# Kernel optimization log

Hardware: AMD Instinct MI355X
Metric: run time of the kernel (lower is better)

Reference implementation:

```python
import jax, jax.numpy as jnp
import numpy as np

N_NODES = 100000
IN_F = 128
H_F = 128
LOOKBACK = 3
N_EDGES = 640000


def setup_inputs() -> dict:
    key = jax.random.key(0)
    ks = jax.random.split(key, 16)
    s = lambda k, shp: jax.random.normal(k, shp, dtype=jnp.float32) * 0.05
    inp = {
        "feat": jax.random.normal(ks[0], (N_NODES, IN_F), dtype=jnp.float32),
        "edges": jax.random.randint(ks[1], (LOOKBACK, 2, N_EDGES), 0, N_NODES, dtype=jnp.int32),
        # conv1 (SAGEConv pool, in->h) params
        "Wp1": s(ks[2], (IN_F, IN_F)), "bp1": jnp.zeros((IN_F,), jnp.float32),
        "Ws1": s(ks[3], (H_F, IN_F)), "Wn1": s(ks[4], (H_F, IN_F)), "b1": jnp.zeros((H_F,), jnp.float32),
        # BatchNorm1d affine params (training-mode batch stats)
        "gamma": jnp.ones((H_F,), jnp.float32), "beta": jnp.zeros((H_F,), jnp.float32),
        # conv2 (SAGEConv pool, h->h) params
        "Wp2": s(ks[5], (H_F, H_F)), "bp2": jnp.zeros((H_F,), jnp.float32),
        "Ws2": s(ks[6], (H_F, H_F)), "Wn2": s(ks[7], (H_F, H_F)), "b2": jnp.zeros((H_F,), jnp.float32),
    }
    return inp


def _sage_pool_conv(h, src, dst, Wp, bp, Ws, Wn, b):
    # pool aggregator: m = relu(fc_pool(h)); neigh = max over in-edges
    m = jax.nn.relu(h @ Wp.T + bp)                      # [N, d]
    agg = jax.ops.segment_max(m[src], dst, num_segments=N_NODES)  # [N, d]
    agg = jnp.where(jnp.isfinite(agg), agg, 0.0)        # nodes with no in-edges -> 0
    return h @ Ws.T + agg @ Wn.T + b


def _batchnorm(x, gamma, beta, eps=1e-5):
    mu = jnp.mean(x, axis=0)
    var = jnp.var(x, axis=0)
    return (x - mu) * jax.lax.rsqrt(var + eps) * gamma + beta


def reference(feat, edges, Wp1, bp1, Ws1, Wn1, b1, gamma, beta, Wp2, bp2, Ws2, Wn2, b2):
    def per_graph(e):
        src, dst = e[0], e[1]
        h = _sage_pool_conv(feat, src, dst, Wp1, bp1, Ws1, Wn1, b1)
        h = _batchnorm(h, gamma, beta)
        h = jax.nn.relu(h)
        h = _sage_pool_conv(h, src, dst, Wp2, bp2, Ws2, Wn2, b2)
        return h

    return jax.vmap(per_graph)(edges)  # [lookback, N, H_F]
```

## Files before the change

### kernel.cpp

```cpp
#include <hip/hip_runtime.h>
#include <hip/hip_bf16.h>

#define NNODES 100000
#define FD 128
#define NEDGES 640000
#define NB 391
#define GRID64 1563
#define OFFS_U32 100032
#define BNRED 64

typedef __bf16 bf16x8 __attribute__((ext_vector_type(8)));
typedef __bf16 bf16x4 __attribute__((ext_vector_type(4)));
typedef float f32x4 __attribute__((ext_vector_type(4)));
typedef unsigned short u16x8 __attribute__((ext_vector_type(8)));

__device__ __forceinline__ bf16x8 cvt8(float4 a, float4 b) {
  bf16x8 r;
  r[0] = (__bf16)a.x; r[1] = (__bf16)a.y; r[2] = (__bf16)a.z; r[3] = (__bf16)a.w;
  r[4] = (__bf16)b.x; r[5] = (__bf16)b.y; r[6] = (__bf16)b.z; r[7] = (__bf16)b.w;
  return r;
}

__device__ __forceinline__ void gl16(const void* g, void* l) {
  __builtin_amdgcn_global_load_lds(
      (const __attribute__((address_space(1))) unsigned int*)g,
      (__attribute__((address_space(3))) unsigned int*)l, 16, 0, 0);
}

__device__ __forceinline__ void stage_w32(const __bf16* Wp, char* l, int tid) {
  const int wid = tid >> 6, lane = tid & 63;
#pragma unroll
  for (int i = 0; i < 8; ++i) {
    const int off = (wid * 8 + i) * 1024;
    gl16((const char*)Wp + off + lane * 16, l + off);
  }
}

__device__ __forceinline__ void stage_abf(const __bf16* A, long row0, int M,
                                          char* l, int tid) {
  const int wid = tid >> 6;
  long row = row0 + (tid & 63);
  if (row > M - 1) row = M - 1;
  const char* base = (const char*)(A + row * FD);
#pragma unroll
  for (int i = 0; i < 4; ++i) {
    const int s = wid * 4 + i;
    gl16(base + s * 16, l + s * 1024);
  }
}

__global__ __launch_bounds__(256) void packw6_k(
    const float* __restrict__ W0, const float* __restrict__ W1,
    const float* __restrict__ W2, const float* __restrict__ W3,
    const float* __restrict__ W4, const float* __restrict__ W5,
    __bf16* __restrict__ out) {
  const int gidx = blockIdx.x * 256 + threadIdx.x;
  const int wi = gidx >> 11;
  const int f = gidx & 2047;
  const float* W = wi == 0 ? W0 : wi == 1 ? W1 : wi == 2 ? W2
                 : wi == 3 ? W3 : wi == 4 ? W4 : W5;
  const int c = f >> 8, kk = (f >> 6) & 3, lane = f & 63;
  const int lr = lane & 15, lg = lane >> 4;
  const float* p = W + (c * 16 + lr) * FD + kk * 32 + lg * 8;
  *(bf16x8*)(out + (long)gidx * 8) = cvt8(*(const float4*)p, *(const float4*)(p + 4));
}

__device__ __forceinline__ void glb_arow32(const float* A, long row, int kbase,
                                           bf16x8 (&af)[4]) {
#pragma unroll
  for (int kk = 0; kk < 4; ++kk) {
    const float* ap = A + row * FD + kbase + kk * 32;
    af[kk] = cvt8(*(const float4*)ap, *(const float4*)(ap + 4));
  }
}

template <int AM>
__device__ __forceinline__ void lds_abf(const char* l, int rl, int lg,
                                        const float* __restrict__ scsh,
                                        bf16x8 (&af)[4]) {
#pragma unroll
  for (int kk = 0; kk < 4; ++kk) {
    const bf16x8 r = *(const bf16x8*)(l + (kk * 4 + lg) * 1024 + rl * 16);
    if constexpr (AM == 3) {
      const int k = lg * 8 + kk * 32;
      const float4 scx = *(const float4*)(scsh + k);
      const float4 scy = *(const float4*)(scsh + k + 4);
      const float4 shx = *(const float4*)(scsh + 128 + k);
      const float4 shy = *(const float4*)(scsh + 128 + k + 4);
      bf16x8 o;
      o[0] = (__bf16)fmaxf((float)r[0] * scx.x + shx.x, 0.f);
      o[1] = (__bf16)fmaxf((float)r[1] * scx.y + shx.y, 0.f);
      o[2] = (__bf16)fmaxf((float)r[2] * scx.z + shx.z, 0.f);
      o[3] = (__bf16)fmaxf((float)r[3] * scx.w + shx.w, 0.f);
      o[4] = (__bf16)fmaxf((float)r[4] * scy.x + shy.x, 0.f);
      o[5] = (__bf16)fmaxf((float)r[5] * scy.y + shy.y, 0.f);
      o[6] = (__bf16)fmaxf((float)r[6] * scy.z + shy.z, 0.f);
      o[7] = (__bf16)fmaxf((float)r[7] * scy.w + shy.w, 0.f);
      af[kk] = o;
    } else {
      af[kk] = r;
    }
  }
}

template <int A0M, int A1M, bool TWOA, bool RELU, bool OUTBF16, bool STATS, bool WRITEB>
__global__ __launch_bounds__(256, 2) void gemm_k(
    const void* __restrict__ A0, long a0s, const void* __restrict__ A1, long a1s,
    const __bf16* __restrict__ W0p, const __bf16* __restrict__ W1p,
    const float* __restrict__ bias, const float* __restrict__ scsh0,
    void* __restrict__ outp, long os, float* __restrict__ pblk,
    __bf16* __restrict__ bcopy, int M) {
  constexpr int LSZ = TWOA ? 65536 : (A0M == 0 ? 32768 : 49152);
  __shared__ __align__(16) char lds[LSZ];
  char* lW0 = lds;
  char* lA0 = lds + 32768;
  char* lA1 = lds + 49152;
  char* lW1 = lds + 32768;

  const int g = blockIdx.y;
  const int tid = threadIdx.x;
  const int wid = tid >> 6;
  const int lane = tid & 63;
  const int rw = wid & 1;
  const int cw = wid >> 1;
  const int lr = lane & 15;
  const int lg = lane >> 4;
  const long row0 = (long)blockIdx.x * 64;

  const void* A0g = (const char*)A0 + (long)g * a0s;
  const void* A1g = (const char*)A1 + (TWOA ? (long)g * a1s : 0);
  void* outg = (char*)outp + (long)g * os;
  const float* scshg = (A0M == 3 || A1M == 3) ? scsh0 + (long)g * 256 : nullptr;

  stage_w32(W0p, lW0, tid);
  if constexpr (A0M != 0) stage_abf((const __bf16*)A0g, row0, M, lA0, tid);
  if constexpr (TWOA) stage_abf((const __bf16*)A1g, row0, M, lA1, tid);
  __syncthreads();

  bf16x8 a0[2][4];
  bf16x8 a1[2][4];
  if constexpr (A0M == 0) {
#pragma unroll
    for (int t = 0; t < 2; ++t) {
      long row = row0 + rw * 32 + t * 16 + lr;
      if (row > M - 1) row = M - 1;
      glb_arow32((const float*)A0g, row, lg * 8, a0[t]);
    }
  } else {
#pragma unroll
    for (int t = 0; t < 2; ++t)
      lds_abf<A0M>(lA0, rw * 32 + t * 16 + lr, lg, scshg, a0[t]);
  }
  if constexpr (TWOA) {
#pragma unroll
    for (int t = 0; t < 2; ++t)
      lds_abf<A1M>(lA1, rw * 32 + t * 16 + lr, lg, scshg, a1[t]);
    __syncthreads();
    stage_w32(W1p, lW1, tid);
  }

  if constexpr (WRITEB) {
    if (cw == 0) {
#pragma unroll
      for (int t = 0; t < 2; ++t) {
        const long row = row0 + rw * 32 + t * 16 + lr;
        if (row < M)
#pragma unroll
          for (int kk = 0; kk < 4; ++kk)
            *(bf16x8*)(bcopy + row * FD + lg * 8 + kk * 32) = a0[t][kk];
      }
    }
  }

  f32x4 acc[2][4];
#pragma unroll
  for (int t = 0; t < 2; ++t)
#pragma unroll
    for (int ci = 0; ci < 4; ++ci) acc[t][ci] = (f32x4){0.f, 0.f, 0.f, 0.f};

#pragma unroll
  for (int ci = 0; ci < 4; ++ci) {
    bf16x8 bw[4];
#pragma unroll
    for (int kk = 0; kk < 4; ++kk)
      bw[kk] = *(const bf16x8*)(lW0 + ((cw * 4 + ci) * 4 + kk) * 1024 + lane * 16);
#pragma unroll
    for (int t = 0; t < 2; ++t)
#pragma unroll
      for (int kk = 0; kk < 4; ++kk)
        acc[t][ci] = __builtin_amdgcn_mfma_f32_16x16x32_bf16(bw[kk], a0[t][kk], acc[t][ci], 0, 0, 0);
  }
  if constexpr (TWOA) {
    __syncthreads();
#pragma unroll
    for (int ci = 0; ci < 4; ++ci) {
      bf16x8 bw[4];
#pragma unroll
      for (int kk = 0; kk < 4; ++kk)
        bw[kk] = *(const bf16x8*)(lW1 + ((cw * 4 + ci) * 4 + kk) * 1024 + lane * 16);
#pragma unroll
      for (int t = 0; t < 2; ++t)
#pragma unroll
        for (int kk = 0; kk < 4; ++kk)
          acc[t][ci] = __builtin_amdgcn_mfma_f32_16x16x32_bf16(bw[kk], a1[t][kk], acc[t][ci], 0, 0, 0);
    }
  }

  float ps[4][4], pss[4][4];
  if constexpr (STATS) {
#pragma unroll
    for (int ci = 0; ci < 4; ++ci)
#pragma unroll
      for (int j = 0; j < 4; ++j) { ps[ci][j] = 0.f; pss[ci][j] = 0.f; }
  }

#pragma unroll
  for (int t = 0; t < 2; ++t) {
    const long row = row0 + rw * 32 + t * 16 + lr;
    const bool ok = row < M;
#pragma unroll
    for (int ci = 0; ci < 4; ++ci) {
      const int cb = cw * 64 + ci * 16 + lg * 4;
      f32x4 v = acc[t][ci];
      if (bias) {
        const float4 bv = *(const float4*)(bias + cb);
        v[0] += bv.x; v[1] += bv.y; v[2] += bv.z; v[3] += bv.w;
      }
      if constexpr (STATS) {
        if (ok) {
#pragma unroll
          for (int j = 0; j < 4; ++j) { ps[ci][j] += v[j]; pss[ci][j] += v[j] * v[j]; }
        }
      }
      if constexpr (RELU) {
#pragma unroll
        for (int j = 0; j < 4; ++j) v[j] = fmaxf(v[j], 0.f);
      }
      if (ok) {
        if constexpr (OUTBF16) {
          bf16x4 o;
          o[0] = (__bf16)v[0]; o[1] = (__bf16)v[1];
          o[2] = (__bf16)v[2]; o[3] = (__bf16)v[3];
          *(bf16x4*)((__bf16*)outg + row * FD + cb) = o;
        } else {
          *(f32x4*)((float*)outg + row * FD + cb) = v;
        }
      }
    }
  }

  if constexpr (STATS) {
    __shared__ float s_red[2][4][64];
#pragma unroll
    for (int ci = 0; ci < 4; ++ci)
#pragma unroll
      for (int j = 0; j < 4; ++j) {
        float s = ps[ci][j], q = pss[ci][j];
        s += __shfl_xor(s, 1); s += __shfl_xor(s, 2);
        s += __shfl_xor(s, 4); s += __shfl_xor(s, 8);
        q += __shfl_xor(q, 1); q += __shfl_xor(q, 2);
        q += __shfl_xor(q, 4); q += __shfl_xor(q, 8);
        if (lr == 0) {
          s_red[0][wid][ci * 16 + lg * 4 + j] = s;
          s_red[1][wid][ci * 16 + lg * 4 + j] = q;
        }
      }
    __syncthreads();
    const int wh = tid >> 7, cg = tid & 127;
    const int cwi = cg >> 6, cl = cg & 63;
    float* pblkg = pblk + (long)g * ((long)GRID64 * 256);
    pblkg[(long)blockIdx.x * 256 + tid] =
        s_red[wh][cwi * 2 + 0][cl] + s_red[wh][cwi * 2 + 1][cl];
  }
}

__global__ __launch_bounds__(256) void bn_red1_k(const float* __restrict__ pblk,
                                                 float* __restrict__ pblk2) {
  const int g = blockIdx.y;
  const float* p = pblk + (long)g * GRID64 * 256;
  float s = 0.f;
  for (int r = blockIdx.x; r < GRID64; r += BNRED) s += p[(long)r * 256 + threadIdx.x];
  pblk2[((long)g * BNRED + blockIdx.x) * 256 + threadIdx.x] = s;
}

__global__ __launch_bounds__(256) void bn_final2_k(const float* __restrict__ pblk2,
                                                   const float* __restrict__ gamma,
                                                   const float* __restrict__ beta,
                                                   float* __restrict__ scsh3) {
  __shared__ float s_ss[128];
  const int g = blockIdx.y;
  const int tid = threadIdx.x;
  const float* p = pblk2 + (long)g * BNRED * 256;
  float s = 0.f;
#pragma unroll
  for (int r = 0; r < BNRED; ++r) s += p[r * 256 + tid];
  if (tid >= 128) s_ss[tid - 128] = s;
  __syncthreads();
  if (tid < 128) {
    const float mu = s / (float)NNODES;
    const float var = s_ss[tid] / (float)NNODES - mu * mu;
    const float sc = rsqrtf(var + 1e-5f) * gamma[tid];
    scsh3[g * 256 + tid] = sc;
    scsh3[g * 256 + 128 + tid] = beta[tid] - mu * sc;
  }
}


__global__ __launch_bounds__(256) void hist_rank3_k(const int* __restrict__ edges,
                                                    unsigned* __restrict__ deg3,
                                                    unsigned short* __restrict__ rank3) {
  const int g = blockIdx.y;
  const int e = blockIdx.x * 256 + threadIdx.x;
  if (e < NEDGES) {
    const int d = edges[(long)g * 2 * NEDGES + NEDGES + e];
    const unsigned r = atomicAdd(&deg3[(long)g * NNODES + d], 1u);
    rank3[(long)g * NEDGES + e] = (unsigned short)r;
  }
}

__global__ __launch_bounds__(256) void blocksum3_k(const unsigned* __restrict__ deg3,
                                                   unsigned* __restrict__ bsum3) {
  __shared__ unsigned s[256];
  const int g = blockIdx.y;
  const int i = blockIdx.x * 256 + threadIdx.x;
  s[threadIdx.x] = (i < NNODES) ? deg3[(long)g * NNODES + i] : 0u;
  __syncthreads();
#pragma unroll
  for (int o = 128; o > 0; o >>= 1) {
    if (threadIdx.x < o) s[threadIdx.x] += s[threadIdx.x + o];
    __syncthreads();
  }
  if (threadIdx.x == 0) bsum3[g * NB + blockIdx.x] = s[0];
}

__global__ __launch_bounds__(512) void scanb3_k(const unsigned* __restrict__ bsum3,
                                                unsigned* __restrict__ boffs3,
                                                unsigned* __restrict__ offs3) {
  __shared__ unsigned s[512];
  const int g = blockIdx.y;
  const unsigned v = (threadIdx.x < NB) ? bsum3[g * NB + threadIdx.x] : 0u;
  s[threadIdx.x] = v;
  __syncthreads();
#pragma unroll
  for (int o = 1; o < 512; o <<= 1) {
    unsigned t = (threadIdx.x >= o) ? s[threadIdx.x - o] : 0u;
    __syncthreads();
    s[threadIdx.x] += t;
    __syncthreads();
  }
  if (threadIdx.x < NB) boffs3[g * NB + threadIdx.x] = s[threadIdx.x] - v;
  if (threadIdx.x == 0) offs3[(long)g * OFFS_U32 + NNODES] = NEDGES;
}

__global__ __launch_bounds__(256) void offsets3_k(const unsigned* __restrict__ deg3,
                                                  const unsigned* __restrict__ boffs3,
                                                  unsigned* __restrict__ offs3) {
  __shared__ unsigned s[256];
  const int g = blockIdx.y;
  const int i = blockIdx.x * 256 + threadIdx.x;
  const unsigned v = (i < NNODES) ? deg3[(long)g * NNODES + i] : 0u;
  s[threadIdx.x] = v;
  __syncthreads();
#pragma unroll
  for (int o = 1; o < 256; o <<= 1) {
    unsigned t = (threadIdx.x >= o) ? s[threadIdx.x - o] : 0u;
    __syncthreads();
    s[threadIdx.x] += t;
    __syncthreads();
  }
  const unsigned excl = s[threadIdx.x] - v + boffs3[g * NB + blockIdx.x];
  if (i < NNODES) offs3[(long)g * OFFS_U32 + i] = excl;
}

__global__ __launch_bounds__(256) void scat3_k(const int* __restrict__ edges,
                                               const unsigned* __restrict__ offs3,
                                               const unsigned short* __restrict__ rank3,
                                               int* __restrict__ ssrc3) {
  const int g = blockIdx.y;
  const int e = blockIdx.x * 256 + threadIdx.x;
  if (e < NEDGES) {
    const int s = edges[(long)g * 2 * NEDGES + e];
    const int d = edges[(long)g * 2 * NEDGES + NEDGES + e];
    const unsigned p = offs3[(long)g * OFFS_U32 + d] + rank3[(long)g * NEDGES + e];
    ssrc3[(long)g * NEDGES + p] = s;
  }
}

__global__ __launch_bounds__(256) void agg_k(const unsigned short* __restrict__ m,
                                             long ms, const int* __restrict__ ssrc3,
                                             const unsigned* __restrict__ offs3,
                                             unsigned short* __restrict__ agg3) {
  const int g = blockIdx.y;
  const unsigned short* mg = m + (long)g * ms;
  const int* ssrc = ssrc3 + (long)g * NEDGES;
  const unsigned* offs = offs3 + (long)g * OFFS_U32;
  unsigned short* agg = agg3 + (long)g * NNODES * FD;

  const int gid = blockIdx.x * 256 + threadIdx.x;
  const int node = gid >> 4;
  if (node >= NNODES) return;
  const int fl = (gid & 15) * 8;
  const unsigned beg = offs[node], end = offs[node + 1];
  u16x8 acc = {0, 0, 0, 0, 0, 0, 0, 0};
  unsigned i = beg;
  for (; i + 2 <= end; i += 2) {
    const int s0 = ssrc[i];
    const int s1 = ssrc[i + 1];
    const u16x8 v0 = *(const u16x8*)(mg + (long)s0 * FD + fl);
    const u16x8 v1 = *(const u16x8*)(mg + (long)s1 * FD + fl);
#pragma unroll
    for (int j = 0; j < 8; ++j) {
      const unsigned short mx = v0[j] > v1[j] ? v0[j] : v1[j];
      acc[j] = mx > acc[j] ? mx : acc[j];
    }
  }
  if (i < end) {
    const u16x8 v = *(const u16x8*)(mg + (long)ssrc[i] * FD + fl);
#pragma unroll
    for (int j = 0; j < 8; ++j) acc[j] = v[j] > acc[j] ? v[j] : acc[j];
  }
  *(u16x8*)(agg + (long)node * FD + fl) = acc;
}

__global__ __launch_bounds__(256) void zero_k(float4* __restrict__ p, long n4) {
  const long i = (long)blockIdx.x * 256 + threadIdx.x;
  if (i < n4) p[i] = (float4){0.f, 0.f, 0.f, 0.f};
}

extern "C" void kernel_launch(void* const* d_in, const int* in_sizes, int n_in,
                              void* d_out, int out_size, void* d_ws, size_t ws_size,
                              hipStream_t stream) {
  const float* feat = (const float*)d_in[0];
  const int* edges = (const int*)d_in[1];
  const float* Wp1 = (const float*)d_in[2];
  const float* bp1 = (const float*)d_in[3];
  const float* Ws1 = (const float*)d_in[4];
  const float* Wn1 = (const float*)d_in[5];
  const float* b1 = (const float*)d_in[6];
  const float* gamma = (const float*)d_in[7];
  const float* beta = (const float*)d_in[8];
  const float* Wp2 = (const float*)d_in[9];
  const float* bp2 = (const float*)d_in[10];
  const float* Ws2 = (const float*)d_in[11];
  const float* Wn2 = (const float*)d_in[12];
  const float* b2 = (const float*)d_in[13];

  const long SZ_BF = 25600000;
  const long SZ_F32 = 51200000;

  char* w = (char*)d_ws;
  __bf16* m1 = (__bf16*)w;
  __bf16* featb = (__bf16*)(w + 25600000);
  __bf16* h1b3 = (__bf16*)(w + 51200000);
  __bf16* aggb3 = (__bf16*)(w + 128000000);
  __bf16* m2_3 = (__bf16*)(w + 204800000);
  float* pblk3 = (float*)(w + 204800000);
  float* pblk2_3 = (float*)(w + 209700096);
  __bf16* wpk = (__bf16*)(w + 281600000);
  float* scsh3 = (float*)(w + 281796608);
  unsigned* deg3 = (unsigned*)(w + 281799680);
  unsigned* offs3 = (unsigned*)(w + 282999680);
  unsigned* bsum3 = (unsigned*)(w + 284200064);
  unsigned* boffs3 = (unsigned*)(w + 284204928);
  unsigned short* rank3 = (unsigned short*)(w + 284209792);
  int* ssrc3 = (int*)(w + 288049792);

  __bf16* Wp1p = wpk;
  __bf16* Ws1p = wpk + 16384;
  __bf16* Wn1p = wpk + 2 * 16384;
  __bf16* Wp2p = wpk + 3 * 16384;
  __bf16* Ws2p = wpk + 4 * 16384;
  __bf16* Wn2p = wpk + 5 * 16384;

  const dim3 blk(256);
  const int edgeGrid = (NEDGES + 255) / 256;
  const int aggGrid = (NNODES * 16 + 255) / 256;
  const int degZeroGrid = (3 * NNODES / 4 + 255) / 256;

  packw6_k<<<48, blk, 0, stream>>>(Wp1, Ws1, Wn1, Wp2, Ws2, Wn2, wpk);

  zero_k<<<degZeroGrid, blk, 0, stream>>>((float4*)deg3, 3L * NNODES / 4);
  hist_rank3_k<<<dim3(edgeGrid, 3), blk, 0, stream>>>(edges, deg3, rank3);
  blocksum3_k<<<dim3(NB, 3), blk, 0, stream>>>(deg3, bsum3);
  scanb3_k<<<dim3(1, 3), dim3(512), 0, stream>>>(bsum3, boffs3, offs3);
  offsets3_k<<<dim3(NB, 3), blk, 0, stream>>>(deg3, boffs3, offs3);
  scat3_k<<<dim3(edgeGrid, 3), blk, 0, stream>>>(edges, offs3, rank3, ssrc3);

  gemm_k<0, 0, false, true, true, false, true><<<dim3(GRID64, 1), blk, 0, stream>>>(
      feat, 0, nullptr, 0, Wp1p, nullptr, bp1, nullptr, m1, 0, nullptr, featb, NNODES);

  agg_k<<<dim3(aggGrid, 3), blk, 0, stream>>>((const unsigned short*)m1, 0L,
                                              ssrc3, offs3, (unsigned short*)aggb3);
  gemm_k<1, 1, true, false, true, true, false><<<dim3(GRID64, 3), blk, 0, stream>>>(
      aggb3, SZ_BF, featb, 0, Wn1p, Ws1p, b1, nullptr, h1b3, SZ_BF, pblk3, nullptr, NNODES);
  bn_red1_k<<<dim3(BNRED, 3), blk, 0, stream>>>(pblk3, pblk2_3);
  bn_final2_k<<<dim3(1, 3), blk, 0, stream>>>(pblk2_3, gamma, beta, scsh3);

  gemm_k<3, 0, false, true, true, false, false><<<dim3(GRID64, 3), blk, 0, stream>>>(
      h1b3, SZ_BF, nullptr, 0, Wp2p, nullptr, bp2, scsh3, m2_3, SZ_BF, nullptr, nullptr, NNODES);
  agg_k<<<dim3(aggGrid, 3), blk, 0, stream>>>((const unsigned short*)m2_3,
                                              (long)NNODES * FD, ssrc3, offs3,
                                              (unsigned short*)aggb3);
  gemm_k<3, 1, true, false, false, false, false><<<dim3(GRID64, 3), blk, 0, stream>>>(
      h1b3, SZ_BF, aggb3, SZ_BF, Ws2p, Wn2p, b2, scsh3, d_out, SZ_F32, nullptr, nullptr, NNODES);
}
```

Before: 556.9 us.

## Make GEMM kernels persistent with double-buffered A tiles and resident weights

The GEMM kernels become persistent 512-thread blocks. Each block stages the weights into LDS once and then loops over 64-row tiles with a grid stride, prefetching the next A tile into a second LDS buffer via global_load_lds while computing the current one. The head GEMM now stages fp32 features through LDS rather than loading them straight from global memory. With fewer blocks, the BatchNorm partial sums come from 85 blocks per graph and the intermediate reduction kernel is removed. The cost is a large LDS footprint at one block per CU and a barrier on every tile.

```diff
diff --git a/kernel.cpp b/kernel.cpp
--- a/kernel.cpp
+++ b/kernel.cpp
@@ -5,9 +5,11 @@
 #define FD 128
 #define NEDGES 640000
 #define NB 391
-#define GRID64 1563
+#define NT64 1563
+#define GX_TWOA 85
+#define GX_ONEW 170
+#define GX_HEAD 255
 #define OFFS_U32 100032
-#define BNRED 64
 
 typedef __bf16 bf16x8 __attribute__((ext_vector_type(8)));
 typedef __bf16 bf16x4 __attribute__((ext_vector_type(4)));
@@ -27,19 +29,29 @@
       (__attribute__((address_space(3))) unsigned int*)l, 16, 0, 0);
 }
 
-__device__ __forceinline__ void stage_w32(const __bf16* Wp, char* l, int tid) {
-  const int wid = tid >> 6, lane = tid & 63;
-#pragma unroll
-  for (int i = 0; i < 8; ++i) {
-    const int off = (wid * 8 + i) * 1024;
+__device__ __forceinline__ void stage_w32(const __bf16* Wp, char* l, int wid, int lane) {
+#pragma unroll
+  for (int i = 0; i < 4; ++i) {
+    const int off = (wid * 4 + i) * 1024;
     gl16((const char*)Wp + off + lane * 16, l + off);
   }
 }
 
 __device__ __forceinline__ void stage_abf(const __bf16* A, long row0, int M,
-                                          char* l, int tid) {
-  const int wid = tid >> 6;
-  long row = row0 + (tid & 63);
+                                          char* l, int wid, int lane) {
+  long row = row0 + lane;
+  if (row > M - 1) row = M - 1;
+  const char* base = (const char*)(A + row * FD);
+#pragma unroll
+  for (int i = 0; i < 2; ++i) {
+    const int s = wid * 2 + i;
+    gl16(base + s * 16, l + s * 1024);
+  }
+}
+
+__device__ __forceinline__ void stage_a32(const float* A, long row0, int M,
+                                          char* l, int wid, int lane) {
+  long row = row0 + lane;
   if (row > M - 1) row = M - 1;
   const char* base = (const char*)(A + row * FD);
 #pragma unroll
@@ -65,163 +77,141 @@
   *(bf16x8*)(out + (long)gidx * 8) = cvt8(*(const float4*)p, *(const float4*)(p + 4));
 }
 
-__device__ __forceinline__ void glb_arow32(const float* A, long row, int kbase,
-                                           bf16x8 (&af)[4]) {
+template <int AM>
+__device__ __forceinline__ void lds_arow(const char* l, int rl, int lg,
+                                         const float* __restrict__ scsh,
+                                         bf16x8 (&af)[4]) {
 #pragma unroll
   for (int kk = 0; kk < 4; ++kk) {
-    const float* ap = A + row * FD + kbase + kk * 32;
-    af[kk] = cvt8(*(const float4*)ap, *(const float4*)(ap + 4));
-  }
-}
-
-template <int AM>
-__device__ __forceinline__ void lds_abf(const char* l, int rl, int lg,
-                                        const float* __restrict__ scsh,
-                                        bf16x8 (&af)[4]) {
-#pragma unroll
-  for (int kk = 0; kk < 4; ++kk) {
-    const bf16x8 r = *(const bf16x8*)(l + (kk * 4 + lg) * 1024 + rl * 16);
-    if constexpr (AM == 3) {
-      const int k = lg * 8 + kk * 32;
-      const float4 scx = *(const float4*)(scsh + k);
-      const float4 scy = *(const float4*)(scsh + k + 4);
-      const float4 shx = *(const float4*)(scsh + 128 + k);
-      const float4 shy = *(const float4*)(scsh + 128 + k + 4);
-      bf16x8 o;
-      o[0] = (__bf16)fmaxf((float)r[0] * scx.x + shx.x, 0.f);
-      o[1] = (__bf16)fmaxf((float)r[1] * scx.y + shx.y, 0.f);
-      o[2] = (__bf16)fmaxf((float)r[2] * scx.z + shx.z, 0.f);
-      o[3] = (__bf16)fmaxf((float)r[3] * scx.w + shx.w, 0.f);
-      o[4] = (__bf16)fmaxf((float)r[4] * scy.x + shy.x, 0.f);
-      o[5] = (__bf16)fmaxf((float)r[5] * scy.y + shy.y, 0.f);
-      o[6] = (__bf16)fmaxf((float)r[6] * scy.z + shy.z, 0.f);
-      o[7] = (__bf16)fmaxf((float)r[7] * scy.w + shy.w, 0.f);
-      af[kk] = o;
+    if constexpr (AM == 0) {
+      const int s = kk * 8 + lg * 2;
+      const float4 x = *(const float4*)(l + s * 1024 + rl * 16);
+      const float4 y = *(const float4*)(l + (s + 1) * 1024 + rl * 16);
+      af[kk] = cvt8(x, y);
     } else {
-      af[kk] = r;
+      const bf16x8 r = *(const bf16x8*)(l + (kk * 4 + lg) * 1024 + rl * 16);
+      if constexpr (AM == 3) {
+        const int k = lg * 8 + kk * 32;
+        const float4 scx = *(const float4*)(scsh + k);
+        const float4 scy = *(const float4*)(scsh + k + 4);
+        const float4 shx = *(const float4*)(scsh + 128 + k);
+        const float4 shy = *(const float4*)(scsh + 128 + k + 4);
+        bf16x8 o;
+        o[0] = (__bf16)fmaxf((float)r[0] * scx.x + shx.x, 0.f);
+        o[1] = (__bf16)fmaxf((float)r[1] * scx.y + shx.y, 0.f);
+        o[2] = (__bf16)fmaxf((float)r[2] * scx.z + shx.z, 0.f);
+        o[3] = (__bf16)fmaxf((float)r[3] * scx.w + shx.w, 0.f);
+        o[4] = (__bf16)fmaxf((float)r[4] * scy.x + shy.x, 0.f);
+        o[5] = (__bf16)fmaxf((float)r[5] * scy.y + shy.y, 0.f);
+        o[6] = (__bf16)fmaxf((float)r[6] * scy.z + shy.z, 0.f);
+        o[7] = (__bf16)fmaxf((float)r[7] * scy.w + shy.w, 0.f);
+        af[kk] = o;
+      } else {
+        af[kk] = r;
+      }
     }
   }
 }
 
 template <int A0M, int A1M, bool TWOA, bool RELU, bool OUTBF16, bool STATS, bool WRITEB>
-__global__ __launch_bounds__(256, 2) void gemm_k(
+__global__ __launch_bounds__(512, 1) void gemm_k(
     const void* __restrict__ A0, long a0s, const void* __restrict__ A1, long a1s,
     const __bf16* __restrict__ W0p, const __bf16* __restrict__ W1p,
     const float* __restrict__ bias, const float* __restrict__ scsh0,
     void* __restrict__ outp, long os, float* __restrict__ pblk,
     __bf16* __restrict__ bcopy, int M) {
-  constexpr int LSZ = TWOA ? 65536 : (A0M == 0 ? 32768 : 49152);
+  constexpr int WSZ = TWOA ? 65536 : 32768;
+  constexpr int ASZ = (A0M == 0) ? 32768 : 16384;
+  constexpr int A1SZ = TWOA ? 16384 : 0;
+  constexpr int LSZ = WSZ + 2 * (ASZ + A1SZ) + (STATS ? 4096 : 0);
   __shared__ __align__(16) char lds[LSZ];
   char* lW0 = lds;
-  char* lA0 = lds + 32768;
-  char* lA1 = lds + 49152;
   char* lW1 = lds + 32768;
+  char* lA0a = lds + WSZ;
+  char* lA1a = lds + WSZ + ASZ;
+  char* lA0b = lds + WSZ + ASZ + A1SZ;
+  char* lA1b = lds + WSZ + ASZ + A1SZ + ASZ;
+  float* s_red = (float*)(lds + WSZ + 2 * (ASZ + A1SZ));
 
   const int g = blockIdx.y;
   const int tid = threadIdx.x;
   const int wid = tid >> 6;
   const int lane = tid & 63;
-  const int rw = wid & 1;
-  const int cw = wid >> 1;
+  const int rw = wid & 3;
+  const int cw = wid >> 2;
   const int lr = lane & 15;
   const int lg = lane >> 4;
-  const long row0 = (long)blockIdx.x * 64;
+  const int S = gridDim.x;
 
   const void* A0g = (const char*)A0 + (long)g * a0s;
   const void* A1g = (const char*)A1 + (TWOA ? (long)g * a1s : 0);
   void* outg = (char*)outp + (long)g * os;
   const float* scshg = (A0M == 3 || A1M == 3) ? scsh0 + (long)g * 256 : nullptr;
 
-  stage_w32(W0p, lW0, tid);
-  if constexpr (A0M != 0) stage_abf((const __bf16*)A0g, row0, M, lA0, tid);
-  if constexpr (TWOA) stage_abf((const __bf16*)A1g, row0, M, lA1, tid);
-  __syncthreads();
-
-  bf16x8 a0[2][4];
-  bf16x8 a1[2][4];
-  if constexpr (A0M == 0) {
-#pragma unroll
-    for (int t = 0; t < 2; ++t) {
-      long row = row0 + rw * 32 + t * 16 + lr;
-      if (row > M - 1) row = M - 1;
-      glb_arow32((const float*)A0g, row, lg * 8, a0[t]);
-    }
-  } else {
-#pragma unroll
-    for (int t = 0; t < 2; ++t)
-      lds_abf<A0M>(lA0, rw * 32 + t * 16 + lr, lg, scshg, a0[t]);
-  }
-  if constexpr (TWOA) {
-#pragma unroll
-    for (int t = 0; t < 2; ++t)
-      lds_abf<A1M>(lA1, rw * 32 + t * 16 + lr, lg, scshg, a1[t]);
-    __syncthreads();
-    stage_w32(W1p, lW1, tid);
-  }
-
-  if constexpr (WRITEB) {
-    if (cw == 0) {
-#pragma unroll
-      for (int t = 0; t < 2; ++t) {
-        const long row = row0 + rw * 32 + t * 16 + lr;
-        if (row < M)
-#pragma unroll
-          for (int kk = 0; kk < 4; ++kk)
-            *(bf16x8*)(bcopy + row * FD + lg * 8 + kk * 32) = a0[t][kk];
-      }
-    }
-  }
-
-  f32x4 acc[2][4];
-#pragma unroll
-  for (int t = 0; t < 2; ++t)
-#pragma unroll
-    for (int ci = 0; ci < 4; ++ci) acc[t][ci] = (f32x4){0.f, 0.f, 0.f, 0.f};
-
-#pragma unroll
-  for (int ci = 0; ci < 4; ++ci) {
-    bf16x8 bw[4];
-#pragma unroll
-    for (int kk = 0; kk < 4; ++kk)
-      bw[kk] = *(const bf16x8*)(lW0 + ((cw * 4 + ci) * 4 + kk) * 1024 + lane * 16);
-#pragma unroll
-    for (int t = 0; t < 2; ++t)
-#pragma unroll
-      for (int kk = 0; kk < 4; ++kk)
-        acc[t][ci] = __builtin_amdgcn_mfma_f32_16x16x32_bf16(bw[kk], a0[t][kk], acc[t][ci], 0, 0, 0);
-  }
-  if constexpr (TWOA) {
-    __syncthreads();
+  float ps[4][4], pss[4][4];
+  if constexpr (STATS) {
+#pragma unroll
+    for (int ci = 0; ci < 4; ++ci)
+#pragma unroll
+      for (int j = 0; j < 4; ++j) { ps[ci][j] = 0.f; pss[ci][j] = 0.f; }
+  }
+
+  auto stageA = [&](long t, char* la0, char* la1) {
+    if constexpr (A0M == 0) stage_a32((const float*)A0g, t * 64, M, la0, wid, lane);
+    else stage_abf((const __bf16*)A0g, t * 64, M, la0, wid, lane);
+    if constexpr (TWOA) stage_abf((const __bf16*)A1g, t * 64, M, la1, wid, lane);
+  };
+
+  auto body = [&](long t, long tn, char* la0, char* la1, char* na0, char* na1) {
+    if (tn < NT64) stageA(tn, na0, na1);
+    const int rl = rw * 16 + lr;
+    const long row = t * 64 + rl;
+    const bool ok = row < M;
+
+    bf16x8 a0f[4];
+    lds_arow<A0M>(la0, rl, lg, scshg, a0f);
+    bf16x8 a1f[4];
+    if constexpr (TWOA) lds_arow<A1M>(la1, rl, lg, scshg, a1f);
+
+    if constexpr (WRITEB) {
+      if (cw == 0 && ok) {
+#pragma unroll
+        for (int kk = 0; kk < 4; ++kk)
+          *(bf16x8*)(bcopy + row * FD + lg * 8 + kk * 32) = a0f[kk];
+      }
+    }
+
+    f32x4 acc[4];
+#pragma unroll
+    for (int ci = 0; ci < 4; ++ci) acc[ci] = (f32x4){0.f, 0.f, 0.f, 0.f};
+
 #pragma unroll
     for (int ci = 0; ci < 4; ++ci) {
       bf16x8 bw[4];
 #pragma unroll
       for (int kk = 0; kk < 4; ++kk)
-        bw[kk] = *(const bf16x8*)(lW1 + ((cw * 4 + ci) * 4 + kk) * 1024 + lane * 16);
-#pragma unroll
-      for (int t = 0; t < 2; ++t)
+        bw[kk] = *(const bf16x8*)(lW0 + ((cw * 4 + ci) * 4 + kk) * 1024 + lane * 16);
+#pragma unroll
+      for (int kk = 0; kk < 4; ++kk)
+        acc[ci] = __builtin_amdgcn_mfma_f32_16x16x32_bf16(bw[kk], a0f[kk], acc[ci], 0, 0, 0);
+    }
+    if constexpr (TWOA) {
+#pragma unroll
+      for (int ci = 0; ci < 4; ++ci) {
+        bf16x8 bw[4];
 #pragma unroll
         for (int kk = 0; kk < 4; ++kk)
-          acc[t][ci] = __builtin_amdgcn_mfma_f32_16x16x32_bf16(bw[kk], a1[t][kk], acc[t][ci], 0, 0, 0);
-    }
-  }
-
-  float ps[4][4], pss[4][4];
-  if constexpr (STATS) {
-#pragma unroll
-    for (int ci = 0; ci < 4; ++ci)
-#pragma unroll
-      for (int j = 0; j < 4; ++j) { ps[ci][j] = 0.f; pss[ci][j] = 0.f; }
-  }
-
-#pragma unroll
-  for (int t = 0; t < 2; ++t) {
-    const long row = row0 + rw * 32 + t * 16 + lr;
-    const bool ok = row < M;
+          bw[kk] = *(const bf16x8*)(lW1 + ((cw * 4 + ci) * 4 + kk) * 1024 + lane * 16);
+#pragma unroll
+        for (int kk = 0; kk < 4; ++kk)
+          acc[ci] = __builtin_amdgcn_mfma_f32_16x16x32_bf16(bw[kk], a1f[kk], acc[ci], 0, 0, 0);
+      }
+    }
+
 #pragma unroll
     for (int ci = 0; ci < 4; ++ci) {
       const int cb = cw * 64 + ci * 16 + lg * 4;
-      f32x4 v = acc[t][ci];
+      f32x4 v = acc[ci];
       if (bias) {
         const float4 bv = *(const float4*)(bias + cb);
         v[0] += bv.x; v[1] += bv.y; v[2] += bv.z; v[3] += bv.w;
@@ -247,10 +237,27 @@
         }
       }
     }
+    __syncthreads();
+  };
+
+  stage_w32(W0p, lW0, wid, lane);
+  if constexpr (TWOA) stage_w32(W1p, lW1, wid, lane);
+  long t = blockIdx.x;
+  stageA(t, lA0a, lA1a);
+  __syncthreads();
+
+  for (;;) {
+    long tn = t + S;
+    body(t, tn, lA0a, lA1a, lA0b, lA1b);
+    t = tn;
+    if (t >= NT64) break;
+    tn = t + S;
+    body(t, tn, lA0b, lA1b, lA0a, lA1a);
+    t = tn;
+    if (t >= NT64) break;
   }
 
   if constexpr (STATS) {
-    __shared__ float s_red[2][4][64];
 #pragma unroll
     for (int ci = 0; ci < 4; ++ci)
 #pragma unroll
@@ -261,39 +268,32 @@
         q += __shfl_xor(q, 1); q += __shfl_xor(q, 2);
         q += __shfl_xor(q, 4); q += __shfl_xor(q, 8);
         if (lr == 0) {
-          s_red[0][wid][ci * 16 + lg * 4 + j] = s;
-          s_red[1][wid][ci * 16 + lg * 4 + j] = q;
+          s_red[(0 * 8 + wid) * 64 + ci * 16 + lg * 4 + j] = s;
+          s_red[(1 * 8 + wid) * 64 + ci * 16 + lg * 4 + j] = q;
         }
       }
     __syncthreads();
-    const int wh = tid >> 7, cg = tid & 127;
-    const int cwi = cg >> 6, cl = cg & 63;
-    float* pblkg = pblk + (long)g * ((long)GRID64 * 256);
-    pblkg[(long)blockIdx.x * 256 + tid] =
-        s_red[wh][cwi * 2 + 0][cl] + s_red[wh][cwi * 2 + 1][cl];
-  }
-}
-
-__global__ __launch_bounds__(256) void bn_red1_k(const float* __restrict__ pblk,
-                                                 float* __restrict__ pblk2) {
-  const int g = blockIdx.y;
-  const float* p = pblk + (long)g * GRID64 * 256;
-  float s = 0.f;
-  for (int r = blockIdx.x; r < GRID64; r += BNRED) s += p[(long)r * 256 + threadIdx.x];
-  pblk2[((long)g * BNRED + blockIdx.x) * 256 + threadIdx.x] = s;
-}
-
-__global__ __launch_bounds__(256) void bn_final2_k(const float* __restrict__ pblk2,
+    if (tid < 256) {
+      const int which = tid >> 7, col = tid & 127;
+      const int cwi = col >> 6, cl = col & 63;
+      float a = 0.f;
+#pragma unroll
+      for (int r = 0; r < 4; ++r) a += s_red[(which * 8 + cwi * 4 + r) * 64 + cl];
+      pblk[((long)g * gridDim.x + blockIdx.x) * 256 + tid] = a;
+    }
+  }
+}
+
+__global__ __launch_bounds__(256) void bn_final2_k(const float* __restrict__ pblk,
                                                    const float* __restrict__ gamma,
                                                    const float* __restrict__ beta,
                                                    float* __restrict__ scsh3) {
   __shared__ float s_ss[128];
   const int g = blockIdx.y;
   const int tid = threadIdx.x;
-  const float* p = pblk2 + (long)g * BNRED * 256;
+  const float* p = pblk + (long)g * GX_TWOA * 256;
   float s = 0.f;
-#pragma unroll
-  for (int r = 0; r < BNRED; ++r) s += p[r * 256 + tid];
+  for (int r = 0; r < GX_TWOA; ++r) s += p[r * 256 + tid];
   if (tid >= 128) s_ss[tid - 128] = s;
   __syncthreads();
   if (tid < 128) {
@@ -455,7 +455,6 @@
   __bf16* aggb3 = (__bf16*)(w + 128000000);
   __bf16* m2_3 = (__bf16*)(w + 204800000);
   float* pblk3 = (float*)(w + 204800000);
-  float* pblk2_3 = (float*)(w + 209700096);
   __bf16* wpk = (__bf16*)(w + 281600000);
   float* scsh3 = (float*)(w + 281796608);
   unsigned* deg3 = (unsigned*)(w + 281799680);
@@ -473,6 +472,7 @@
   __bf16* Wn2p = wpk + 5 * 16384;
 
   const dim3 blk(256);
+  const dim3 blk512(512);
   const int edgeGrid = (NEDGES + 255) / 256;
   const int aggGrid = (NNODES * 16 + 255) / 256;
   const int degZeroGrid = (3 * NNODES / 4 + 255) / 256;
@@ -486,21 +486,20 @@
   offsets3_k<<<dim3(NB, 3), blk, 0, stream>>>(deg3, boffs3, offs3);
   scat3_k<<<dim3(edgeGrid, 3), blk, 0, stream>>>(edges, offs3, rank3, ssrc3);
 
-  gemm_k<0, 0, false, true, true, false, true><<<dim3(GRID64, 1), blk, 0, stream>>>(
+  gemm_k<0, 0, false, true, true, false, true><<<dim3(GX_HEAD, 1), blk512, 0, stream>>>(
       feat, 0, nullptr, 0, Wp1p, nullptr, bp1, nullptr, m1, 0, nullptr, featb, NNODES);
 
   agg_k<<<dim3(aggGrid, 3), blk, 0, stream>>>((const unsigned short*)m1, 0L,
                                               ssrc3, offs3, (unsigned short*)aggb3);
-  gemm_k<1, 1, true, false, true, true, false><<<dim3(GRID64, 3), blk, 0, stream>>>(
+  gemm_k<1, 1, true, false, true, true, false><<<dim3(GX_TWOA, 3), blk512, 0, stream>>>(
       aggb3, SZ_BF, featb, 0, Wn1p, Ws1p, b1, nullptr, h1b3, SZ_BF, pblk3, nullptr, NNODES);
-  bn_red1_k<<<dim3(BNRED, 3), blk, 0, stream>>>(pblk3, pblk2_3);
-  bn_final2_k<<<dim3(1, 3), blk, 0, stream>>>(pblk2_3, gamma, beta, scsh3);
-
-  gemm_k<3, 0, false, true, true, false, false><<<dim3(GRID64, 3), blk, 0, stream>>>(
+  bn_final2_k<<<dim3(1, 3), blk, 0, stream>>>(pblk3, gamma, beta, scsh3);
+
+  gemm_k<3, 0, false, true, true, false, false><<<dim3(GX_ONEW, 3), blk512, 0, stream>>>(
       h1b3, SZ_BF, nullptr, 0, Wp2p, nullptr, bp2, scsh3, m2_3, SZ_BF, nullptr, nullptr, NNODES);
   agg_k<<<dim3(aggGrid, 3), blk, 0, stream>>>((const unsigned short*)m2_3,
                                               (long)NNODES * FD, ssrc3, offs3,
                                               (unsigned short*)aggb3);
-  gemm_k<3, 1, true, false, false, false, false><<<dim3(GRID64, 3), blk, 0, stream>>>(
+  gemm_k<3, 1, true, false, false, false, false><<<dim3(GX_TWOA, 3), blk512, 0, stream>>>(
       h1b3, SZ_BF, aggb3, SZ_BF, Ws2p, Wn2p, b2, scsh3, d_out, SZ_F32, nullptr, nullptr, NNODES);
 }
```

Measured after the change: 519.0 us. -6.8%, faster.
